# Optimization experiments

Measured on AMD Instinct MI355X. Metric: run time of the kernel, lower is better.

## Reference

```python
import jax, jax.numpy as jnp
import numpy as np

H = 8  # num_heads

def setup_inputs() -> dict:
    key = jax.random.key(0)
    ks = jax.random.split(key, 8)
    N, B, E = 1024, 8, 256
    value = jax.random.normal(ks[0], (N, B, E), dtype=jnp.float32)
    pos = jax.random.normal(ks[1], (B * H, N, N), dtype=jnp.float32)
    s = 1.0 / np.sqrt(E)
    in_proj_w = jax.random.uniform(ks[2], (3 * E, E), jnp.float32, -s, s)   # content attn qkv proj
    in_proj_b = jnp.zeros((3 * E,), jnp.float32)
    out_w = jax.random.uniform(ks[3], (E, E), jnp.float32, -s, s)
    out_b = jnp.zeros((E,), jnp.float32)
    return {"value": value, "position_attention_weights": pos,
            "in_proj_w": in_proj_w, "in_proj_b": in_proj_b,
            "out_w": out_w, "out_b": out_b}

def reference(value, position_attention_weights, in_proj_w, in_proj_b, out_w, out_b):
    # value: (N, B, E) seq-first, position_attention_weights: (B*H, N, N)
    N, B, E = value.shape
    Dh = E // H
    qkv = value @ in_proj_w.T + in_proj_b            # (N, B, 3E)
    q, k, v = jnp.split(qkv, 3, axis=-1)
    # (N, B, E) -> (B*H, N, Dh)
    def to_heads(t):
        return t.reshape(N, B * H, Dh).transpose(1, 0, 2)
    q, k, v = to_heads(q), to_heads(k), to_heads(v)
    scale = 1.0 / jnp.sqrt(jnp.asarray(Dh, q.dtype))
    content = jnp.einsum('bnd,bmd->bnm', q * scale, k)   # (B*H, N, N) content scores
    # merge_attention == 'gate': clamp both, log-sigmoid gate on positional, add
    content = jnp.clip(content, -10.0, 10.0)
    pos = jnp.clip(position_attention_weights, -10.0, 10.0)
    scores = jax.nn.log_sigmoid(pos) + content
    attn = jax.nn.softmax(scores, axis=-1)               # normalizer
    out = jnp.einsum('bnm,bmd->bnd', attn, v)            # (B*H, N, Dh)
    out = out.transpose(1, 0, 2).reshape(N, B, E)        # back to (N, B, E)
    out = out @ out_w.T + out_b
    attn_avg = attn.reshape(B, H, N, N).mean(axis=1)     # averaged attention weights
    return out, attn_avg
```

## Files before the change

kernel.cpp:

```cpp
#include <hip/hip_runtime.h>
#include <hip/hip_bf16.h>

typedef __attribute__((ext_vector_type(8))) short short8;
typedef __attribute__((ext_vector_type(4))) float f32x4;
typedef __attribute__((ext_vector_type(4))) unsigned short u16x4;

#define MFMA16(a,b,c) __builtin_amdgcn_mfma_f32_16x16x32_bf16((a),(b),(c),0,0,0)

__device__ __forceinline__ ushort f2bf(float x) {
  union { float f; unsigned u; } v; v.f = x;
  unsigned u = v.u;
  u = (u + 0x7fffu + ((u >> 16) & 1u)) >> 16;
  return (ushort)u;
}

__device__ __forceinline__ float bf2f(ushort u) {
  union { unsigned u; float f; } v; v.u = ((unsigned)u) << 16;
  return v.f;
}

__device__ __forceinline__ short8 ld8(const ushort* p) {
  return *reinterpret_cast<const short8*>(p);
}

__device__ __forceinline__ void glds16(const float* g, float* l) {
  __builtin_amdgcn_global_load_lds(
      (const __attribute__((address_space(1))) unsigned int*)g,
      (__attribute__((address_space(3))) unsigned int*)(void*)l, 16, 0, 0);
}

__global__ void conv_kernel(const float* __restrict__ value,
                            const float* __restrict__ w_in,
                            const float* __restrict__ w_out,
                            ushort* __restrict__ vbf,
                            ushort* __restrict__ wbf,
                            ushort* __restrict__ owbf) {
  int i = blockIdx.x * 256 + threadIdx.x;
  const float* src; ushort* dst; int j;
  if (i < 524288)      { src = value; dst = vbf;  j = i; }
  else if (i < 573440) { src = w_in;  dst = wbf;  j = i - 524288; }
  else                 { src = w_out; dst = owbf; j = i - 573440; }
  float4 v = reinterpret_cast<const float4*>(src)[j];
  u16x4 o;
  o[0] = f2bf(v.x); o[1] = f2bf(v.y); o[2] = f2bf(v.z); o[3] = f2bf(v.w);
  reinterpret_cast<u16x4*>(dst)[j] = o;
}

__global__ __launch_bounds__(256) void qkv_kernel(
    const ushort* __restrict__ vbf, const ushort* __restrict__ wbf,
    const float* __restrict__ bias,
    ushort* __restrict__ qh, ushort* __restrict__ kh, ushort* __restrict__ vv) {
  int tid = threadIdx.x;
  int wave = tid >> 6, lane = tid & 63;
  int lq = lane & 15, lg = lane >> 4;
  int r0 = blockIdx.x * 16;
  int c0 = (blockIdx.y * 4 + wave) * 16;
  f32x4 acc = {0.f, 0.f, 0.f, 0.f};
  const ushort* ap = vbf + (size_t)(r0 + lq) * 256 + lg * 8;
  const ushort* bp = wbf + (size_t)(c0 + lq) * 256 + lg * 8;
#pragma unroll
  for (int k0 = 0; k0 < 256; k0 += 32)
    acc = MFMA16(ld8(ap + k0), ld8(bp + k0), acc);
  int c = c0 + lq;
  float bv = bias[c];
#pragma unroll
  for (int r = 0; r < 4; ++r) {
    int row = r0 + lg * 4 + r;
    int n = row >> 3, b = row & 7;
    float v = acc[r] + bv;
    if (c < 256) {
      int h = c >> 5, d = c & 31;
      qh[((size_t)(b * 8 + h) * 1024 + n) * 32 + d] = f2bf(v * 0.17677669529663689f);
    } else if (c < 512) {
      int cc = c - 256, h = cc >> 5, d = cc & 31;
      kh[((size_t)(b * 8 + h) * 1024 + n) * 32 + d] = f2bf(v);
    } else {
      int cc = c - 512, h = cc >> 5, d = cc & 31;
      vv[((size_t)(b * 8 + h) * 1024 + n) * 32 + d] = f2bf(v);
    }
  }
}

__global__ __launch_bounds__(256) void vtrans_kernel(const ushort* __restrict__ vv,
                                                     ushort* __restrict__ vt) {
  __shared__ ushort t[32][73];
  int tid = threadIdx.x;
  int bh = blockIdx.y, m0 = blockIdx.x * 64;
  int mm = tid >> 2, d0 = (tid & 3) * 8;
  short8 v = ld8(vv + ((size_t)bh * 1024 + m0 + mm) * 32 + d0);
#pragma unroll
  for (int j = 0; j < 8; ++j) t[d0 + j][mm] = (ushort)v[j];
  __syncthreads();
  int d = tid >> 3, mg = (tid & 7) * 8;
  short8 o;
#pragma unroll
  for (int j = 0; j < 8; ++j) o[j] = (short)t[d][mg + j];
  *reinterpret_cast<short8*>(vt + ((size_t)bh * 32 + d) * 1024 + m0 + mg) = o;
}

__global__ __launch_bounds__(512, 2) void attn_kernel(
    const ushort* __restrict__ qh, const ushort* __restrict__ kh,
    const ushort* __restrict__ vt, const float* __restrict__ pos,
    ushort* __restrict__ ao, float* __restrict__ avg_out) {
  __shared__ __align__(16) float pos_lds[2][16][516];
  __shared__ __align__(16) ushort attn_lds[16][1032];
  __shared__ __align__(16) float pvred[8][16][32];
  __shared__ float rowsumT[16][8];

  int tid = threadIdx.x;
  int wave = tid >> 6, lane = tid & 63;
  int lq = lane & 15, lg = lane >> 4;
  int n0 = blockIdx.x * 16;
  int b = blockIdx.y;

  auto stage = [&](int s) {
    int buf = s & 1;
    const float* gb = pos + ((size_t)(b * 8 + (s >> 1)) << 20)
                          + (size_t)n0 * 1024 + (s & 1) * 512;
    int r = wave * 2;
    glds16(gb + (size_t)r * 1024 +       lane * 4, &pos_lds[buf][r][0]);
    glds16(gb + (size_t)r * 1024 + 256 + lane * 4, &pos_lds[buf][r][256]);
    glds16(gb + (size_t)(r + 1) * 1024 +       lane * 4, &pos_lds[buf][r + 1][0]);
    glds16(gb + (size_t)(r + 1) * 1024 + 256 + lane * 4, &pos_lds[buf][r + 1][256]);
  };

  float avg[8][4];
#pragma unroll
  for (int j = 0; j < 8; ++j)
#pragma unroll
    for (int r = 0; r < 4; ++r) avg[j][r] = 0.f;

  stage(0);
  stage(1);
  __syncthreads();

  for (int h = 0; h < 8; ++h) {
    int bh = b * 8 + h;
    const ushort* kp = kh + (size_t)bh * 32768;
    const ushort* vp = vt + (size_t)bh * 32768;
    short8 qa = ld8(qh + ((size_t)bh * 1024 + n0 + lq) * 32 + lg * 8);
    f32x4 acc0 = {0.f, 0.f, 0.f, 0.f}, acc1 = {0.f, 0.f, 0.f, 0.f};
    float rs[4] = {0.f, 0.f, 0.f, 0.f};
    u16x4 wA[4], wB[4];

    auto half_body = [&](int hf, u16x4* wv) {
      int buf = (h * 2 + hf) & 1;
      int mwin = hf * 512 + wave * 64;
      int lcol = wave * 64 + lq * 4;
      f32x4 S[4];
#pragma unroll
      for (int t = 0; t < 4; ++t) {
        f32x4 z = {0.f, 0.f, 0.f, 0.f};
        S[t] = MFMA16(qa, ld8(kp + (size_t)(mwin + lq * 4 + t) * 32 + lg * 8), z);
      }
#pragma unroll
      for (int r = 0; r < 4; ++r) {
        int row = lg * 4 + r;
        f32x4 pv = *reinterpret_cast<const f32x4*>(&pos_lds[buf][row][lcol]);
#pragma unroll
        for (int t = 0; t < 4; ++t) {
          float p = fminf(10.f, fmaxf(-10.f, pv[t]));
          float c = fminf(10.f, fmaxf(-10.f, S[t][r]));
          float w = __expf(c - 10.f) * __builtin_amdgcn_rcpf(1.f + __expf(-p));
          rs[r] += w;
          wv[r][t] = f2bf(w);
        }
        int col = (mwin + lq * 4) ^ ((row & 7) << 3);
        *reinterpret_cast<u16x4*>(&attn_lds[row][col]) = wv[r];
      }
#pragma unroll
      for (int ks = 0; ks < 2; ++ks) {
        int sb = mwin + ks * 32;
        int acol = (sb + lg * 8) ^ ((lq & 7) << 3);
        short8 pa = *reinterpret_cast<const short8*>(&attn_lds[lq][acol]);
        acc0 = MFMA16(pa, ld8(vp + (size_t)lq * 1024 + sb + lg * 8), acc0);
        acc1 = MFMA16(pa, ld8(vp + (size_t)(lq + 16) * 1024 + sb + lg * 8), acc1);
      }
    };

    half_body(0, wA);
    __syncthreads();
    if (h * 2 + 2 < 16) stage(h * 2 + 2);
    half_body(1, wB);

#pragma unroll
    for (int r = 0; r < 4; ++r) {
      rs[r] += __shfl_xor(rs[r], 1);
      rs[r] += __shfl_xor(rs[r], 2);
      rs[r] += __shfl_xor(rs[r], 4);
      rs[r] += __shfl_xor(rs[r], 8);
    }
    if (lq == 0) {
#pragma unroll
      for (int r = 0; r < 4; ++r) rowsumT[lg * 4 + r][wave] = rs[r];
    }
#pragma unroll
    for (int r = 0; r < 4; ++r) {
      pvred[wave][lg * 4 + r][lq] = acc0[r];
      pvred[wave][lg * 4 + r][lq + 16] = acc1[r];
    }
    __syncthreads();
    if (h * 2 + 3 < 16) stage(h * 2 + 3);
#pragma unroll
    for (int r = 0; r < 4; ++r) {
      int row = lg * 4 + r;
      float4 a0 = *reinterpret_cast<const float4*>(&rowsumT[row][0]);
      float4 a1 = *reinterpret_cast<const float4*>(&rowsumT[row][4]);
      float invr = __builtin_amdgcn_rcpf(a0.x + a0.y + a0.z + a0.w +
                                         a1.x + a1.y + a1.z + a1.w);
#pragma unroll
      for (int j = 0; j < 4; ++j) avg[j][r] += bf2f(wA[r][j]) * invr;
#pragma unroll
      for (int j = 0; j < 4; ++j) avg[4 + j][r] += bf2f(wB[r][j]) * invr;
    }
    {
      int n = tid >> 5, d = tid & 31;
      float4 a0 = *reinterpret_cast<const float4*>(&rowsumT[n][0]);
      float4 a1 = *reinterpret_cast<const float4*>(&rowsumT[n][4]);
      float invn = __builtin_amdgcn_rcpf(a0.x + a0.y + a0.z + a0.w +
                                         a1.x + a1.y + a1.z + a1.w);
      float s = 0.f;
#pragma unroll
      for (int w = 0; w < 8; ++w) s += pvred[w][n][d];
      ao[((size_t)(n0 + n) * 8 + b) * 256 + h * 32 + d] = f2bf(s * invn);
    }
  }
#pragma unroll
  for (int r = 0; r < 4; ++r) {
    int n = n0 + lg * 4 + r;
    float* op = avg_out + (size_t)b * 1048576 + (size_t)n * 1024;
    f32x4 v0 = {avg[0][r] * 0.125f, avg[1][r] * 0.125f, avg[2][r] * 0.125f, avg[3][r] * 0.125f};
    f32x4 v1 = {avg[4][r] * 0.125f, avg[5][r] * 0.125f, avg[6][r] * 0.125f, avg[7][r] * 0.125f};
    __builtin_nontemporal_store(v0, reinterpret_cast<f32x4*>(op + wave * 64 + lq * 4));
    __builtin_nontemporal_store(v1, reinterpret_cast<f32x4*>(op + 512 + wave * 64 + lq * 4));
  }
}

__global__ __launch_bounds__(256) void oproj_kernel(
    const ushort* __restrict__ ao, const ushort* __restrict__ owbf,
    const float* __restrict__ ob, float* __restrict__ outp) {
  int tid = threadIdx.x;
  int wave = tid >> 6, lane = tid & 63;
  int lq = lane & 15, lg = lane >> 4;
  int r0 = blockIdx.x * 16;
  int c0 = (blockIdx.y * 4 + wave) * 16;
  f32x4 acc = {0.f, 0.f, 0.f, 0.f};
  const ushort* ap = ao + (size_t)(r0 + lq) * 256 + lg * 8;
  const ushort* bp = owbf + (size_t)(c0 + lq) * 256 + lg * 8;
#pragma unroll
  for (int k0 = 0; k0 < 256; k0 += 32)
    acc = MFMA16(ld8(ap + k0), ld8(bp + k0), acc);
  int c = c0 + lq;
  float bv = ob[c];
#pragma unroll
  for (int r = 0; r < 4; ++r) {
    int row = r0 + lg * 4 + r;
    outp[(size_t)row * 256 + c] = acc[r] + bv;
  }
}

extern "C" void kernel_launch(void* const* d_in, const int* in_sizes, int n_in,
                              void* d_out, int out_size, void* d_ws, size_t ws_size,
                              hipStream_t stream) {
  const float* value = (const float*)d_in[0];
  const float* pos   = (const float*)d_in[1];
  const float* w_in  = (const float*)d_in[2];
  const float* b_in  = (const float*)d_in[3];
  const float* w_out = (const float*)d_in[4];
  const float* b_out = (const float*)d_in[5];

  char* ws = (char*)d_ws;
  ushort* vbf  = (ushort*)(ws);
  ushort* wbf  = (ushort*)(ws + 4194304);
  ushort* owbf = (ushort*)(ws + 4587520);
  ushort* qh   = (ushort*)(ws + 4718592);
  ushort* kh   = (ushort*)(ws + 8912896);
  ushort* vv   = (ushort*)(ws + 13107200);
  ushort* vt   = (ushort*)(ws);
  ushort* ao   = (ushort*)(ws + 17301504);

  float* outp = (float*)d_out;
  float* avgp = outp + 2097152;

  conv_kernel<<<2304, 256, 0, stream>>>(value, w_in, w_out, vbf, wbf, owbf);
  qkv_kernel<<<dim3(512, 12), 256, 0, stream>>>(vbf, wbf, b_in, qh, kh, vv);
  vtrans_kernel<<<dim3(16, 64), 256, 0, stream>>>(vv, vt);
  attn_kernel<<<dim3(64, 8), 512, 0, stream>>>(qh, kh, vt, pos, ao, avgp);
  oproj_kernel<<<dim3(512, 4), 256, 0, stream>>>(ao, owbf, b_out, outp);
}
```

Before: 178.8 us.

## Compute transposed score tiles in registers and stream pos directly, dropping LDS staging

```diff
diff --git a/kernel.cpp b/kernel.cpp
--- a/kernel.cpp
+++ b/kernel.cpp
@@ -23,10 +23,8 @@
   return *reinterpret_cast<const short8*>(p);
 }
 
-__device__ __forceinline__ void glds16(const float* g, float* l) {
-  __builtin_amdgcn_global_load_lds(
-      (const __attribute__((address_space(1))) unsigned int*)g,
-      (__attribute__((address_space(3))) unsigned int*)(void*)l, 16, 0, 0);
+__device__ __forceinline__ f32x4 ldnt4(const float* p) {
+  return __builtin_nontemporal_load(reinterpret_cast<const f32x4*>(p));
 }
 
 __global__ void conv_kernel(const float* __restrict__ value,
@@ -98,141 +96,106 @@
   *reinterpret_cast<short8*>(vt + ((size_t)bh * 32 + d) * 1024 + m0 + mg) = o;
 }
 
-__global__ __launch_bounds__(512, 2) void attn_kernel(
+__global__ __launch_bounds__(256, 2) void attn_kernel(
     const ushort* __restrict__ qh, const ushort* __restrict__ kh,
     const ushort* __restrict__ vt, const float* __restrict__ pos,
     ushort* __restrict__ ao, float* __restrict__ avg_out) {
-  __shared__ __align__(16) float pos_lds[2][16][516];
-  __shared__ __align__(16) ushort attn_lds[16][1032];
-  __shared__ __align__(16) float pvred[8][16][32];
-  __shared__ float rowsumT[16][8];
+  __shared__ float pvred[2][4][16][32];
+  __shared__ float rowsumT[2][16][4];
 
   int tid = threadIdx.x;
   int wave = tid >> 6, lane = tid & 63;
   int lq = lane & 15, lg = lane >> 4;
   int n0 = blockIdx.x * 16;
   int b = blockIdx.y;
-
-  auto stage = [&](int s) {
-    int buf = s & 1;
-    const float* gb = pos + ((size_t)(b * 8 + (s >> 1)) << 20)
-                          + (size_t)n0 * 1024 + (s & 1) * 512;
-    int r = wave * 2;
-    glds16(gb + (size_t)r * 1024 +       lane * 4, &pos_lds[buf][r][0]);
-    glds16(gb + (size_t)r * 1024 + 256 + lane * 4, &pos_lds[buf][r][256]);
-    glds16(gb + (size_t)(r + 1) * 1024 +       lane * 4, &pos_lds[buf][r + 1][0]);
-    glds16(gb + (size_t)(r + 1) * 1024 + 256 + lane * 4, &pos_lds[buf][r + 1][256]);
-  };
-
-  float avg[8][4];
-#pragma unroll
-  for (int j = 0; j < 8; ++j)
-#pragma unroll
-    for (int r = 0; r < 4; ++r) avg[j][r] = 0.f;
-
-  stage(0);
-  stage(1);
-  __syncthreads();
+  int wbase = wave * 256;
+  int ra = ((lq >> 2) << 3) + (lq & 3);
+
+  float avg[8][8];
+#pragma unroll
+  for (int u = 0; u < 8; ++u)
+#pragma unroll
+    for (int i = 0; i < 8; ++i) avg[u][i] = 0.f;
 
   for (int h = 0; h < 8; ++h) {
     int bh = b * 8 + h;
     const ushort* kp = kh + (size_t)bh * 32768;
     const ushort* vp = vt + (size_t)bh * 32768;
+    const float* ppr = pos + ((size_t)bh << 20) + (size_t)(n0 + lq) * 1024 + wbase;
     short8 qa = ld8(qh + ((size_t)bh * 1024 + n0 + lq) * 32 + lg * 8);
+
     f32x4 acc0 = {0.f, 0.f, 0.f, 0.f}, acc1 = {0.f, 0.f, 0.f, 0.f};
-    float rs[4] = {0.f, 0.f, 0.f, 0.f};
-    u16x4 wA[4], wB[4];
-
-    auto half_body = [&](int hf, u16x4* wv) {
-      int buf = (h * 2 + hf) & 1;
-      int mwin = hf * 512 + wave * 64;
-      int lcol = wave * 64 + lq * 4;
-      f32x4 S[4];
-#pragma unroll
-      for (int t = 0; t < 4; ++t) {
-        f32x4 z = {0.f, 0.f, 0.f, 0.f};
-        S[t] = MFMA16(qa, ld8(kp + (size_t)(mwin + lq * 4 + t) * 32 + lg * 8), z);
+    float rs = 0.f;
+    short8 wh[8];
+
+#pragma unroll
+    for (int u = 0; u < 8; ++u) {
+      int mu = wbase + u * 32;
+      short8 ka = ld8(kp + (size_t)(mu + ra) * 32 + lg * 8);
+      short8 kb = ld8(kp + (size_t)(mu + ra + 4) * 32 + lg * 8);
+      f32x4 p0 = ldnt4(ppr + u * 32 + lg * 8);
+      f32x4 p1 = ldnt4(ppr + u * 32 + lg * 8 + 4);
+      f32x4 z = {0.f, 0.f, 0.f, 0.f};
+      f32x4 SA = MFMA16(ka, qa, z);
+      f32x4 SB = MFMA16(kb, qa, z);
+      short8 w8;
+#pragma unroll
+      for (int i = 0; i < 4; ++i) {
+        float p = fminf(10.f, fmaxf(-10.f, p0[i]));
+        float c = fminf(10.f, fmaxf(-10.f, SA[i]));
+        float w = __expf(c - 10.f) * __builtin_amdgcn_rcpf(1.f + __expf(-p));
+        rs += w;
+        w8[i] = (short)f2bf(w);
       }
 #pragma unroll
-      for (int r = 0; r < 4; ++r) {
-        int row = lg * 4 + r;
-        f32x4 pv = *reinterpret_cast<const f32x4*>(&pos_lds[buf][row][lcol]);
-#pragma unroll
-        for (int t = 0; t < 4; ++t) {
-          float p = fminf(10.f, fmaxf(-10.f, pv[t]));
-          float c = fminf(10.f, fmaxf(-10.f, S[t][r]));
-          float w = __expf(c - 10.f) * __builtin_amdgcn_rcpf(1.f + __expf(-p));
-          rs[r] += w;
-          wv[r][t] = f2bf(w);
-        }
-        int col = (mwin + lq * 4) ^ ((row & 7) << 3);
-        *reinterpret_cast<u16x4*>(&attn_lds[row][col]) = wv[r];
+      for (int i = 0; i < 4; ++i) {
+        float p = fminf(10.f, fmaxf(-10.f, p1[i]));
+        float c = fminf(10.f, fmaxf(-10.f, SB[i]));
+        float w = __expf(c - 10.f) * __builtin_amdgcn_rcpf(1.f + __expf(-p));
+        rs += w;
+        w8[4 + i] = (short)f2bf(w);
       }
-#pragma unroll
-      for (int ks = 0; ks < 2; ++ks) {
-        int sb = mwin + ks * 32;
-        int acol = (sb + lg * 8) ^ ((lq & 7) << 3);
-        short8 pa = *reinterpret_cast<const short8*>(&attn_lds[lq][acol]);
-        acc0 = MFMA16(pa, ld8(vp + (size_t)lq * 1024 + sb + lg * 8), acc0);
-        acc1 = MFMA16(pa, ld8(vp + (size_t)(lq + 16) * 1024 + sb + lg * 8), acc1);
-      }
-    };
-
-    half_body(0, wA);
+      wh[u] = w8;
+      acc0 = MFMA16(w8, ld8(vp + (size_t)lq * 1024 + mu + lg * 8), acc0);
+      acc1 = MFMA16(w8, ld8(vp + (size_t)(lq + 16) * 1024 + mu + lg * 8), acc1);
+    }
+    rs += __shfl_xor(rs, 16);
+    rs += __shfl_xor(rs, 32);
+    int buf = h & 1;
+    if (lane < 16) rowsumT[buf][lq][wave] = rs;
+#pragma unroll
+    for (int j = 0; j < 4; ++j) {
+      pvred[buf][wave][lg * 4 + j][lq] = acc0[j];
+      pvred[buf][wave][lg * 4 + j][lq + 16] = acc1[j];
+    }
     __syncthreads();
-    if (h * 2 + 2 < 16) stage(h * 2 + 2);
-    half_body(1, wB);
-
-#pragma unroll
-    for (int r = 0; r < 4; ++r) {
-      rs[r] += __shfl_xor(rs[r], 1);
-      rs[r] += __shfl_xor(rs[r], 2);
-      rs[r] += __shfl_xor(rs[r], 4);
-      rs[r] += __shfl_xor(rs[r], 8);
-    }
-    if (lq == 0) {
-#pragma unroll
-      for (int r = 0; r < 4; ++r) rowsumT[lg * 4 + r][wave] = rs[r];
-    }
-#pragma unroll
-    for (int r = 0; r < 4; ++r) {
-      pvred[wave][lg * 4 + r][lq] = acc0[r];
-      pvred[wave][lg * 4 + r][lq + 16] = acc1[r];
-    }
-    __syncthreads();
-    if (h * 2 + 3 < 16) stage(h * 2 + 3);
-#pragma unroll
-    for (int r = 0; r < 4; ++r) {
-      int row = lg * 4 + r;
-      float4 a0 = *reinterpret_cast<const float4*>(&rowsumT[row][0]);
-      float4 a1 = *reinterpret_cast<const float4*>(&rowsumT[row][4]);
-      float invr = __builtin_amdgcn_rcpf(a0.x + a0.y + a0.z + a0.w +
-                                         a1.x + a1.y + a1.z + a1.w);
-#pragma unroll
-      for (int j = 0; j < 4; ++j) avg[j][r] += bf2f(wA[r][j]) * invr;
-#pragma unroll
-      for (int j = 0; j < 4; ++j) avg[4 + j][r] += bf2f(wB[r][j]) * invr;
-    }
     {
-      int n = tid >> 5, d = tid & 31;
-      float4 a0 = *reinterpret_cast<const float4*>(&rowsumT[n][0]);
-      float4 a1 = *reinterpret_cast<const float4*>(&rowsumT[n][4]);
-      float invn = __builtin_amdgcn_rcpf(a0.x + a0.y + a0.z + a0.w +
-                                         a1.x + a1.y + a1.z + a1.w);
-      float s = 0.f;
-#pragma unroll
-      for (int w = 0; w < 8; ++w) s += pvred[w][n][d];
-      ao[((size_t)(n0 + n) * 8 + b) * 256 + h * 32 + d] = f2bf(s * invn);
-    }
-  }
-#pragma unroll
-  for (int r = 0; r < 4; ++r) {
-    int n = n0 + lg * 4 + r;
-    float* op = avg_out + (size_t)b * 1048576 + (size_t)n * 1024;
-    f32x4 v0 = {avg[0][r] * 0.125f, avg[1][r] * 0.125f, avg[2][r] * 0.125f, avg[3][r] * 0.125f};
-    f32x4 v1 = {avg[4][r] * 0.125f, avg[5][r] * 0.125f, avg[6][r] * 0.125f, avg[7][r] * 0.125f};
-    __builtin_nontemporal_store(v0, reinterpret_cast<f32x4*>(op + wave * 64 + lq * 4));
-    __builtin_nontemporal_store(v1, reinterpret_cast<f32x4*>(op + 512 + wave * 64 + lq * 4));
+      float invr = __builtin_amdgcn_rcpf(rowsumT[buf][lq][0] + rowsumT[buf][lq][1] +
+                                         rowsumT[buf][lq][2] + rowsumT[buf][lq][3]);
+#pragma unroll
+      for (int u = 0; u < 8; ++u)
+#pragma unroll
+        for (int i = 0; i < 8; ++i)
+          avg[u][i] += bf2f((ushort)wh[u][i]) * invr;
+      int n = tid >> 4, d = tid & 15;
+      float invn = __builtin_amdgcn_rcpf(rowsumT[buf][n][0] + rowsumT[buf][n][1] +
+                                         rowsumT[buf][n][2] + rowsumT[buf][n][3]);
+      float s0 = pvred[buf][0][n][d] + pvred[buf][1][n][d] +
+                 pvred[buf][2][n][d] + pvred[buf][3][n][d];
+      float s1 = pvred[buf][0][n][d + 16] + pvred[buf][1][n][d + 16] +
+                 pvred[buf][2][n][d + 16] + pvred[buf][3][n][d + 16];
+      size_t base = ((size_t)(n0 + n) * 8 + b) * 256 + h * 32;
+      ao[base + d] = f2bf(s0 * invn);
+      ao[base + d + 16] = f2bf(s1 * invn);
+    }
+  }
+  float* op = avg_out + (size_t)b * 1048576 + (size_t)(n0 + lq) * 1024 + wbase;
+#pragma unroll
+  for (int u = 0; u < 8; ++u) {
+    f32x4 v0 = {avg[u][0] * 0.125f, avg[u][1] * 0.125f, avg[u][2] * 0.125f, avg[u][3] * 0.125f};
+    f32x4 v1 = {avg[u][4] * 0.125f, avg[u][5] * 0.125f, avg[u][6] * 0.125f, avg[u][7] * 0.125f};
+    __builtin_nontemporal_store(v0, reinterpret_cast<f32x4*>(op + u * 32 + lg * 8));
+    __builtin_nontemporal_store(v1, reinterpret_cast<f32x4*>(op + u * 32 + lg * 8 + 4));
   }
 }
 
@@ -285,6 +248,6 @@
   conv_kernel<<<2304, 256, 0, stream>>>(value, w_in, w_out, vbf, wbf, owbf);
   qkv_kernel<<<dim3(512, 12), 256, 0, stream>>>(vbf, wbf, b_in, qh, kh, vv);
   vtrans_kernel<<<dim3(16, 64), 256, 0, stream>>>(vv, vt);
-  attn_kernel<<<dim3(64, 8), 512, 0, stream>>>(qh, kh, vt, pos, ao, avgp);
+  attn_kernel<<<dim3(64, 8), 256, 0, stream>>>(qh, kh, vt, pos, ao, avgp);
   oproj_kernel<<<dim3(512, 4), 256, 0, stream>>>(ao, owbf, b_out, outp);
 }
```

Result: slower. 197.9 us (+10.7%).
